# Optimization experiments

Hardware: AMD Instinct MI355X
Metric: run time of the kernel (lower is better)

## Reference

```python
import jax, jax.numpy as jnp
import numpy as np

EPS_REG = 0.1     # Sinkhorn regularization eps (init arg)
MAX_ITER = 50     # max Sinkhorn iterations (init arg)
THRESH = 0.1      # early-stop threshold from the torch code

N, P1, P2, D = 4, 2048, 2048, 64


def setup_inputs() -> dict:
    key = jax.random.key(0)
    k1, k2, k3 = jax.random.split(key, 3)
    x = jax.random.normal(k1, (N, P1, D), dtype=jnp.float32)
    y = jax.random.normal(k2, (N, P2, D), dtype=jnp.float32)
    M = jax.random.normal(k3, (D, D), dtype=jnp.float32)
    return {"x": x, "y": y, "M": M}


def _cost_matrix(x, y, M):
    # C_ij = (x_i - y_j) M (x_i - y_j)^T, expanded to avoid the [N,P1,P2,D]
    # difference tensor the torch code materializes (identical math):
    #   C = x M x^T (diag) + y M y^T (diag) - x M y^T - (y M x^T)^T
    xM = jnp.einsum('npd,de->npe', x, M)
    yM = jnp.einsum('nqd,de->nqe', y, M)
    dx = jnp.einsum('npd,npd->np', xM, x)  # [N,P1]
    dy = jnp.einsum('nqd,nqd->nq', yM, y)  # [N,P2]
    cross = jnp.einsum('npd,nqd->npq', xM, y) + jnp.einsum('nqd,npd->npq', yM, x)
    return dx[:, :, None] + dy[:, None, :] - cross  # [N,P1,P2]


def _bias(C, u, v, eps):
    # M_ij = (-C_ij + u_i + v_j) / eps
    return (-C + u[..., :, None] + v[..., None, :]) / eps


def _sinkhorn(C, eps):
    n, p1, p2 = C.shape
    log_mu = jnp.log(jnp.full((n, p1), 1.0 / p1, C.dtype) + 1e-8)
    log_nu = jnp.log(jnp.full((n, p2), 1.0 / p2, C.dtype) + 1e-8)
    u0 = jnp.zeros((n, p1), C.dtype)
    v0 = jnp.zeros((n, p2), C.dtype)

    def step(carry, _):
        u, v, active = carry
        u1 = u
        u_new = eps * (log_mu - jax.scipy.special.logsumexp(_bias(C, u, v, eps), axis=-1)) + u
        u = jnp.where(active, u_new, u)
        v_new = eps * (log_nu - jax.scipy.special.logsumexp(_bias(C, u, v, eps), axis=-2)) + v
        v = jnp.where(active, v_new, v)
        err = jnp.mean(jnp.sum(jnp.abs(u - u1), axis=-1))
        active = active & (err >= THRESH)  # freeze updates once converged (== torch break)
        return (u, v, active), None

    (u, v, _), _ = jax.lax.scan(step, (u0, v0, jnp.asarray(True)), None, length=MAX_ITER)
    return u, v


def reference(x, y, M):
    eps = EPS_REG
    C = _cost_matrix(x, y, M)
    u, v = _sinkhorn(C, eps)
    pi = jnp.exp(_bias(C, u, v, eps))
    cost = jnp.sum(pi * C, axis=(-2, -1))  # reduction='none' -> shape [N]
    return cost, pi, C
```

## Files before the change

### kernel.cpp

```cpp
#include <hip/hip_runtime.h>
#include <cstdint>
#include <cstddef>

#define NB 4
#define P1 2048
#define P2 2048
#define DD 64
#define ITER 50
#define EPS 0.1f
#define INV_EPS 10.0f
#define THRESH 0.1f
#define LOG_MU -7.6245985f
#define ELOG (-0.76245985f)
#define MU_VAL 0.00048829125f
#define ERRSLOTS 32
#define RP (P2 / 4)
#define PCHUNKS 128

__global__ void prep0(const float* __restrict__ M, float* __restrict__ S,
                      float* __restrict__ errAcc, int* __restrict__ active,
                      float* __restrict__ cost) {
    int t = threadIdx.x;
    for (int k = t; k < DD * DD; k += 256) {
        int d = k >> 6, e = k & 63;
        S[k] = M[d * DD + e] + M[e * DD + d];
    }
    for (int k = t; k < ITER * ERRSLOTS; k += 256) errAcc[k] = 0.0f;
    if (t < 64) active[t] = (t == 0) ? 1 : 0;
    if (t < NB) cost[t] = 0.0f;
}

__global__ __launch_bounds__(256) void prep1(const float* __restrict__ x,
                                             const float* __restrict__ y,
                                             const float* __restrict__ S,
                                             float* __restrict__ xS,
                                             float* __restrict__ dx,
                                             float* __restrict__ dy,
                                             float* __restrict__ u,
                                             float* __restrict__ v) {
    __shared__ float Sl[DD * DD];
    int t = threadIdx.x;
    for (int k = t; k < DD * DD; k += 256) Sl[k] = S[k];
    __syncthreads();
    int wave = t >> 6, lane = t & 63;
    int r = blockIdx.x * 4 + wave;
    bool isX = r < NB * P1;
    const float* src = isX ? x : y;
    int rr = isX ? r : r - NB * P1;
    float xv = src[(size_t)rr * DD + lane];
    float acc = 0.0f;
    #pragma unroll
    for (int d = 0; d < DD; ++d) {
        float xd = __shfl(xv, d, 64);
        acc = fmaf(xd, Sl[d * DD + lane], acc);
    }
    float p = acc * xv;
    #pragma unroll
    for (int o = 32; o; o >>= 1) p += __shfl_xor(p, o, 64);
    if (isX) {
        xS[(size_t)rr * DD + lane] = acc;
        if (lane == 0) { dx[rr] = 0.5f * p; u[rr] = 0.0f; }
    } else {
        if (lane == 0) { dy[rr] = 0.5f * p; v[rr] = 0.0f; }
    }
}

__global__ __launch_bounds__(256) void gemmC(const float* __restrict__ xS,
                                             const float* __restrict__ y,
                                             const float* __restrict__ dx,
                                             const float* __restrict__ dy,
                                             float* __restrict__ C) {
    __shared__ float xs[64][68];
    __shared__ float ys[64][68];
    int n = blockIdx.z;
    int i0 = blockIdx.y * 64, j0 = blockIdx.x * 64;
    int t = threadIdx.x;

    #pragma unroll
    for (int k = 0; k < 4; ++k) {
        int f = t + 256 * k;
        int row = f >> 4;
        int c4 = f & 15;
        float4 a = ((const float4*)xS)[((size_t)(n * P1 + i0 + row)) * (DD / 4) + c4];
        xs[4 * c4 + 0][row] = a.x; xs[4 * c4 + 1][row] = a.y;
        xs[4 * c4 + 2][row] = a.z; xs[4 * c4 + 3][row] = a.w;
        float4 b = ((const float4*)y)[((size_t)(n * P2 + j0 + row)) * (DD / 4) + c4];
        ys[4 * c4 + 0][row] = b.x; ys[4 * c4 + 1][row] = b.y;
        ys[4 * c4 + 2][row] = b.z; ys[4 * c4 + 3][row] = b.w;
    }
    __syncthreads();

    int tx = t & 15, ty = t >> 4;
    float acc[4][4] = {};
    #pragma unroll
    for (int e = 0; e < 64; ++e) {
        float4 a = *(const float4*)&xs[e][4 * ty];
        float4 b = *(const float4*)&ys[e][4 * tx];
        acc[0][0] = fmaf(a.x, b.x, acc[0][0]); acc[0][1] = fmaf(a.x, b.y, acc[0][1]);
        acc[0][2] = fmaf(a.x, b.z, acc[0][2]); acc[0][3] = fmaf(a.x, b.w, acc[0][3]);
        acc[1][0] = fmaf(a.y, b.x, acc[1][0]); acc[1][1] = fmaf(a.y, b.y, acc[1][1]);
        acc[1][2] = fmaf(a.y, b.z, acc[1][2]); acc[1][3] = fmaf(a.y, b.w, acc[1][3]);
        acc[2][0] = fmaf(a.z, b.x, acc[2][0]); acc[2][1] = fmaf(a.z, b.y, acc[2][1]);
        acc[2][2] = fmaf(a.z, b.z, acc[2][2]); acc[2][3] = fmaf(a.z, b.w, acc[2][3]);
        acc[3][0] = fmaf(a.w, b.x, acc[3][0]); acc[3][1] = fmaf(a.w, b.y, acc[3][1]);
        acc[3][2] = fmaf(a.w, b.z, acc[3][2]); acc[3][3] = fmaf(a.w, b.w, acc[3][3]);
    }

    int iBase = i0 + ty * 4, jBase = j0 + tx * 4;
    float4 dy4 = *(const float4*)&dy[n * P2 + jBase];
    #pragma unroll
    for (int r = 0; r < 4; ++r) {
        float dxv = dx[n * P1 + iBase + r];
        float4 o;
        o.x = dxv + dy4.x - acc[r][0];
        o.y = dxv + dy4.y - acc[r][1];
        o.z = dxv + dy4.z - acc[r][2];
        o.w = dxv + dy4.w - acc[r][3];
        *(float4*)&C[((size_t)(n * P1 + iBase + r)) * P2 + jBase] = o;
    }
}

__device__ __forceinline__ void load_row8(float4 dst[8], const float4* base, int lane) {
    #pragma unroll
    for (int k = 0; k < 8; ++k) dst[k] = base[lane + 64 * k];
}

__device__ __forceinline__ float row_lse(float4 c[8], float ai, const float* bl, int lane) {
    float m = -3.4e38f;
    #pragma unroll
    for (int k = 0; k < 8; ++k) {
        float4 vv = ((const float4*)bl)[lane + 64 * k];
        c[k].x = (ai - c[k].x) + vv.x;
        c[k].y = (ai - c[k].y) + vv.y;
        c[k].z = (ai - c[k].z) + vv.z;
        c[k].w = (ai - c[k].w) + vv.w;
        m = fmaxf(m, fmaxf(fmaxf(c[k].x, c[k].y), fmaxf(c[k].z, c[k].w)));
    }
    #pragma unroll
    for (int o = 1; o < 64; o <<= 1) m = fmaxf(m, __shfl_xor(m, o, 64));
    float s = 0.0f;
    #pragma unroll
    for (int k = 0; k < 8; ++k)
        s += __expf((c[k].x - m) * INV_EPS) + __expf((c[k].y - m) * INV_EPS) +
             __expf((c[k].z - m) * INV_EPS) + __expf((c[k].w - m) * INV_EPS);
    #pragma unroll
    for (int o = 1; o < 64; o <<= 1) s += __shfl_xor(s, o, 64);
    return EPS * __logf(s) + m;
}

__device__ __forceinline__ void mergec(float& m, float& s, float q) {
    float nm = fmaxf(m, q);
    s = s * __expf((m - nm) * INV_EPS) + __expf((q - nm) * INV_EPS);
    m = nm;
}
__device__ __forceinline__ void mergems(float& m, float& s, float mo, float so) {
    float nm = fmaxf(m, mo);
    s = s * __expf((m - nm) * INV_EPS) + so * __expf((mo - nm) * INV_EPS);
    m = nm;
}
__device__ __forceinline__ void merge44(float4& m, float4& s, float4 mo, float4 so) {
    mergems(m.x, s.x, mo.x, so.x);
    mergems(m.y, s.y, mo.y, so.y);
    mergems(m.z, s.z, mo.z, so.z);
    mergems(m.w, s.w, mo.w, so.w);
}

__device__ __forceinline__ void merge_row(float4 M[8], float4 S[8],
                                          const float4 q[8], float dr) {
    #pragma unroll
    for (int k = 0; k < 8; ++k) {
        mergec(M[k].x, S[k].x, q[k].x + dr);
        mergec(M[k].y, S[k].y, q[k].y + dr);
        mergec(M[k].z, S[k].z, q[k].z + dr);
        mergec(M[k].w, S[k].w, q[k].w + dr);
    }
}

__global__ __launch_bounds__(256) void iter_pass(const float* __restrict__ C,
                                                 float* __restrict__ u,
                                                 const float* __restrict__ v,
                                                 float* __restrict__ pm,
                                                 float* __restrict__ ps,
                                                 float* __restrict__ errAcc,
                                                 const int* __restrict__ active,
                                                 int t_iter) {
    if (!active[t_iter]) return;
    __shared__ float bl[P2];
    __shared__ float4 LM[4][512];
    __shared__ float4 LS[4][512];
    __shared__ float da_s[4];
    int t = threadIdx.x;
    int n = blockIdx.x >> 7;
    int i0 = (blockIdx.x & (PCHUNKS - 1)) * 16;
    {
        const float4* bsrc = (const float4*)(v + n * P2);
        ((float4*)bl)[t] = bsrc[t];
        ((float4*)bl)[t + 256] = bsrc[t + 256];
    }
    __syncthreads();

    int wave = t >> 6, lane = t & 63;
    int irow = i0 + wave * 4;
    float* arow = u + n * P1 + irow;
    float a0 = arow[0], a1 = arow[1], a2 = arow[2], a3 = arow[3];
    const float4* base = (const float4*)(C + ((size_t)(n * P1 + irow)) * P2);

    float4 M[8], S[8];
    #pragma unroll
    for (int k = 0; k < 8; ++k) {
        M[k] = make_float4(-3.4e38f, -3.4e38f, -3.4e38f, -3.4e38f);
        S[k] = make_float4(0.0f, 0.0f, 0.0f, 0.0f);
    }

    float4 A[8], B[8];
    load_row8(A, base, lane);
    load_row8(B, base + RP, lane);
    float l0 = row_lse(A, a0, bl, lane);
    float d0 = ELOG - l0;
    merge_row(M, S, A, d0);
    load_row8(A, base + 2 * RP, lane);
    float l1 = row_lse(B, a1, bl, lane);
    float d1 = ELOG - l1;
    merge_row(M, S, B, d1);
    load_row8(B, base + 3 * RP, lane);
    float l2 = row_lse(A, a2, bl, lane);
    float d2 = ELOG - l2;
    merge_row(M, S, A, d2);
    float l3 = row_lse(B, a3, bl, lane);
    float d3 = ELOG - l3;
    merge_row(M, S, B, d3);

    if (lane == 0) {
        arow[0] = a0 + d0; arow[1] = a1 + d1;
        arow[2] = a2 + d2; arow[3] = a3 + d3;
        da_s[wave] = fabsf(d0) + fabsf(d1) + fabsf(d2) + fabsf(d3);
    }

    #pragma unroll
    for (int k = 0; k < 8; ++k) {
        LM[wave][lane + 64 * k] = M[k];
        LS[wave][lane + 64 * k] = S[k];
    }
    __syncthreads();

    float4* pm4 = (float4*)pm;
    float4* ps4 = (float4*)ps;
    size_t pb4 = (size_t)blockIdx.x * 512;
    #pragma unroll
    for (int sl = 0; sl < 2; ++sl) {
        int slot = t + 256 * sl;
        float4 m = LM[0][slot], s = LS[0][slot];
        merge44(m, s, LM[1][slot], LS[1][slot]);
        merge44(m, s, LM[2][slot], LS[2][slot]);
        merge44(m, s, LM[3][slot], LS[3][slot]);
        pm4[pb4 + slot] = m;
        ps4[pb4 + slot] = s;
    }

    if (t == 0) {
        atomicAdd(&errAcc[t_iter * ERRSLOTS + (blockIdx.x & (ERRSLOTS - 1))],
                  da_s[0] + da_s[1] + da_s[2] + da_s[3]);
    }
}

__global__ __launch_bounds__(256) void v_comb(const float* __restrict__ pm,
                                              const float* __restrict__ ps,
                                              float* __restrict__ v,
                                              const float* __restrict__ errAcc,
                                              int* __restrict__ active,
                                              int t_iter) {
    if (blockIdx.x == 0 && threadIdx.x == 0) {
        float e = 0.0f;
        #pragma unroll
        for (int q = 0; q < ERRSLOTS; ++q) e += errAcc[t_iter * ERRSLOTS + q];
        if (active[t_iter] && (e * 0.25f >= THRESH)) active[t_iter + 1] = 1;
    }
    if (!active[t_iter]) return;
    __shared__ float LMv[4][64];
    __shared__ float LSv[4][64];
    int t = threadIdx.x, wave = t >> 6, lane = t & 63;
    int n = blockIdx.x >> 5;
    int j = ((blockIdx.x & 31) << 6) + lane;
    const float* pmb = pm + ((size_t)(n * PCHUNKS + wave * 32)) * P2 + j;
    const float* psb = ps + ((size_t)(n * PCHUNKS + wave * 32)) * P2 + j;
    float m0 = -3.4e38f, s0 = 0.0f, m1 = -3.4e38f, s1 = 0.0f;
    float m2 = -3.4e38f, s2 = 0.0f, m3 = -3.4e38f, s3 = 0.0f;
    #pragma unroll
    for (int c = 0; c < 32; c += 4) {
        mergems(m0, s0, pmb[(size_t)(c + 0) * P2], psb[(size_t)(c + 0) * P2]);
        mergems(m1, s1, pmb[(size_t)(c + 1) * P2], psb[(size_t)(c + 1) * P2]);
        mergems(m2, s2, pmb[(size_t)(c + 2) * P2], psb[(size_t)(c + 2) * P2]);
        mergems(m3, s3, pmb[(size_t)(c + 3) * P2], psb[(size_t)(c + 3) * P2]);
    }
    mergems(m0, s0, m1, s1);
    mergems(m2, s2, m3, s3);
    mergems(m0, s0, m2, s2);
    LMv[wave][lane] = m0; LSv[wave][lane] = s0;
    __syncthreads();
    if (wave == 0) {
        float m = LMv[0][lane], s = LSv[0][lane];
        mergems(m, s, LMv[1][lane], LSv[1][lane]);
        mergems(m, s, LMv[2][lane], LSv[2][lane]);
        mergems(m, s, LMv[3][lane], LSv[3][lane]);
        float lse = EPS * __logf(s) + m;
        v[n * P2 + j] = v[n * P2 + j] + ELOG - lse;
    }
}

__device__ __forceinline__ float row_sum(float4 c[8], float aiv, const float* bl,
                                         int lane) {
    float s = 0.0f;
    #pragma unroll
    for (int k = 0; k < 8; ++k) {
        float4 vv = ((const float4*)bl)[lane + 64 * k];
        c[k].x = __expf(fmaf(c[k].x, -INV_EPS, aiv + vv.x));
        c[k].y = __expf(fmaf(c[k].y, -INV_EPS, aiv + vv.y));
        c[k].z = __expf(fmaf(c[k].z, -INV_EPS, aiv + vv.z));
        c[k].w = __expf(fmaf(c[k].w, -INV_EPS, aiv + vv.w));
        s += (c[k].x + c[k].y) + (c[k].z + c[k].w);
    }
    #pragma unroll
    for (int o = 1; o < 64; o <<= 1) s += __shfl_xor(s, o, 64);
    return s;
}

__device__ __forceinline__ void acc_row(float4 S[8], const float4 q[8], float ed) {
    #pragma unroll
    for (int k = 0; k < 8; ++k) {
        S[k].x = fmaf(q[k].x, ed, S[k].x);
        S[k].y = fmaf(q[k].y, ed, S[k].y);
        S[k].z = fmaf(q[k].z, ed, S[k].z);
        S[k].w = fmaf(q[k].w, ed, S[k].w);
    }
}

__global__ __launch_bounds__(512) void iter_fast(const float* __restrict__ C,
                                                 float* __restrict__ u,
                                                 const float* __restrict__ v,
                                                 float* __restrict__ ps,
                                                 float* __restrict__ errAcc,
                                                 const int* __restrict__ active,
                                                 int t_iter) {
    if (!active[t_iter]) return;
    __shared__ float bl[P2];
    __shared__ float4 LS[8][512];
    __shared__ float da_s[8];
    int t = threadIdx.x;
    int n = blockIdx.x >> 7;
    int i0 = (blockIdx.x & (PCHUNKS - 1)) * 16;
    {
        const float4* bsrc = (const float4*)(v + n * P2);
        float4 b0 = bsrc[t];
        b0.x *= INV_EPS; b0.y *= INV_EPS; b0.z *= INV_EPS; b0.w *= INV_EPS;
        ((float4*)bl)[t] = b0;
    }
    __syncthreads();

    int wave = t >> 6, lane = t & 63;
    int irow = i0 + wave * 2;
    float* arow = u + n * P1 + irow;
    float a0 = arow[0], a1 = arow[1];
    const float4* base = (const float4*)(C + ((size_t)(n * P1 + irow)) * P2);

    float4 S[8];
    #pragma unroll
    for (int k = 0; k < 8; ++k) S[k] = make_float4(0.0f, 0.0f, 0.0f, 0.0f);

    float4 X[8], Y[8];
    load_row8(X, base, lane);
    load_row8(Y, base + RP, lane);
    float s0 = row_sum(X, a0 * INV_EPS, bl, lane);
    float d0 = ELOG - EPS * __logf(s0);
    acc_row(S, X, __fdividef(MU_VAL, s0));
    float s1 = row_sum(Y, a1 * INV_EPS, bl, lane);
    float d1 = ELOG - EPS * __logf(s1);
    acc_row(S, Y, __fdividef(MU_VAL, s1));

    if (lane == 0) {
        arow[0] = a0 + d0; arow[1] = a1 + d1;
        da_s[wave] = fabsf(d0) + fabsf(d1);
    }

    #pragma unroll
    for (int k = 0; k < 8; ++k) LS[wave][lane + 64 * k] = S[k];
    __syncthreads();

    float4* ps4 = (float4*)ps;
    size_t pb4 = (size_t)blockIdx.x * 512;
    {
        int slot = t;
        float4 x0 = LS[0][slot], x1 = LS[1][slot];
        float4 x2 = LS[2][slot], x3 = LS[3][slot];
        float4 x4 = LS[4][slot], x5 = LS[5][slot];
        float4 x6 = LS[6][slot], x7 = LS[7][slot];
        float4 o;
        o.x = ((x0.x + x1.x) + (x2.x + x3.x)) + ((x4.x + x5.x) + (x6.x + x7.x));
        o.y = ((x0.y + x1.y) + (x2.y + x3.y)) + ((x4.y + x5.y) + (x6.y + x7.y));
        o.z = ((x0.z + x1.z) + (x2.z + x3.z)) + ((x4.z + x5.z) + (x6.z + x7.z));
        o.w = ((x0.w + x1.w) + (x2.w + x3.w)) + ((x4.w + x5.w) + (x6.w + x7.w));
        ps4[pb4 + slot] = o;
    }

    if (t == 0) {
        atomicAdd(&errAcc[t_iter * ERRSLOTS + (blockIdx.x & (ERRSLOTS - 1))],
                  ((da_s[0] + da_s[1]) + (da_s[2] + da_s[3])) +
                  ((da_s[4] + da_s[5]) + (da_s[6] + da_s[7])));
    }
}

__global__ __launch_bounds__(256) void v_fast(const float* __restrict__ ps,
                                              float* __restrict__ v,
                                              const float* __restrict__ errAcc,
                                              int* __restrict__ active,
                                              int t_iter) {
    if (blockIdx.x == 0 && threadIdx.x == 0) {
        float e = 0.0f;
        #pragma unroll
        for (int q = 0; q < ERRSLOTS; ++q) e += errAcc[t_iter * ERRSLOTS + q];
        if (active[t_iter] && (e * 0.25f >= THRESH)) active[t_iter + 1] = 1;
    }
    if (!active[t_iter]) return;
    __shared__ float LSv[4][64];
    int t = threadIdx.x, wave = t >> 6, lane = t & 63;
    int n = blockIdx.x >> 5;
    int j = ((blockIdx.x & 31) << 6) + lane;
    const float* psb = ps + ((size_t)(n * PCHUNKS + wave * 32)) * P2 + j;
    float s0 = 0.0f, s1 = 0.0f, s2 = 0.0f, s3 = 0.0f;
    #pragma unroll
    for (int c = 0; c < 32; c += 4) {
        s0 += psb[(size_t)(c + 0) * P2];
        s1 += psb[(size_t)(c + 1) * P2];
        s2 += psb[(size_t)(c + 2) * P2];
        s3 += psb[(size_t)(c + 3) * P2];
    }
    LSv[wave][lane] = (s0 + s1) + (s2 + s3);
    __syncthreads();
    if (wave == 0) {
        float s = (LSv[0][lane] + LSv[1][lane]) + (LSv[2][lane] + LSv[3][lane]);
        v[n * P2 + j] = v[n * P2 + j] + ELOG - EPS * __logf(s);
    }
}

__device__ __forceinline__ float row_pi(const float4 c[8], float ui, const float* vl,
                                        int lane, float4* prow) {
    float acc = 0.0f;
    #pragma unroll
    for (int k = 0; k < 8; ++k) {
        float4 vv = ((const float4*)vl)[lane + 64 * k];
        float4 p;
        p.x = __expf(((ui - c[k].x) + vv.x) * INV_EPS);
        p.y = __expf(((ui - c[k].y) + vv.y) * INV_EPS);
        p.z = __expf(((ui - c[k].z) + vv.z) * INV_EPS);
        p.w = __expf(((ui - c[k].w) + vv.w) * INV_EPS);
        prow[lane + 64 * k] = p;
        acc += p.x * c[k].x + p.y * c[k].y + p.z * c[k].z + p.w * c[k].w;
    }
    return acc;
}

__global__ __launch_bounds__(512) void final_pass(const float* __restrict__ C,
                                                  const float* __restrict__ u,
                                                  const float* __restrict__ v,
                                                  float* __restrict__ pi,
                                                  float* __restrict__ cost) {
    __shared__ float vl[P2];
    __shared__ float red[8];
    int t = threadIdx.x;
    int n = blockIdx.x >> 7;
    int i0 = (blockIdx.x & 127) * 16;
    {
        const float4* vsrc = (const float4*)(v + n * P2);
        ((float4*)vl)[t] = vsrc[t];
    }
    __syncthreads();

    int wave = t >> 6, lane = t & 63;
    int irow = i0 + wave * 2;
    const float* urow = u + n * P1 + irow;
    float u0 = urow[0], u1 = urow[1];
    const float4* base = (const float4*)(C + ((size_t)(n * P1 + irow)) * P2);
    float4* pbase = (float4*)(pi + ((size_t)(n * P1 + irow)) * P2);

    float4 A[8], B[8];
    load_row8(A, base, lane);
    load_row8(B, base + RP, lane);
    float acc = row_pi(A, u0, vl, lane, pbase);
    acc += row_pi(B, u1, vl, lane, pbase + RP);

    #pragma unroll
    for (int o = 1; o < 64; o <<= 1) acc += __shfl_xor(acc, o, 64);
    if (lane == 0) red[wave] = acc;
    __syncthreads();
    if (t == 0) {
        atomicAdd(&cost[n], ((red[0] + red[1]) + (red[2] + red[3])) +
                            ((red[4] + red[5]) + (red[6] + red[7])));
    }
}

extern "C" void kernel_launch(void* const* d_in, const int* in_sizes, int n_in,
                              void* d_out, int out_size, void* d_ws, size_t ws_size,
                              hipStream_t stream) {
    const float* x = (const float*)d_in[0];
    const float* y = (const float*)d_in[1];
    const float* M = (const float*)d_in[2];
    float* out = (float*)d_out;
    float* cost = out;
    float* pi = out + NB;
    float* C = out + NB + (size_t)NB * P1 * P2;

    float* ws = (float*)d_ws;
    float* S      = ws;
    float* xS     = S + DD * DD;
    float* dx     = xS + (size_t)NB * P1 * DD;
    float* dy     = dx + NB * P1;
    float* u      = dy + NB * P2;
    float* v      = u + NB * P1;
    float* errAcc = v + NB * P2;
    int*   active = (int*)(errAcc + ITER * ERRSLOTS);
    float* ws_end = (float*)(active + 64);

    size_t base_floats = (size_t)(ws_end - ws);
    size_t pmps_floats = 2 * (size_t)NB * PCHUNKS * P2;
    float* pm;
    float* ps;
    if (ws_size >= (base_floats + pmps_floats) * sizeof(float)) {
        pm = ws_end;
        ps = ws_end + pmps_floats / 2;
    } else {
        pm = pi;
        ps = pi + pmps_floats / 2;
    }

    prep0<<<1, 256, 0, stream>>>(M, S, errAcc, active, cost);
    prep1<<<(NB * (P1 + P2)) / 4, 256, 0, stream>>>(x, y, S, xS, dx, dy, u, v);
    gemmC<<<dim3(P2 / 64, P1 / 64, NB), 256, 0, stream>>>(xS, y, dx, dy, C);
    iter_pass<<<NB * PCHUNKS, 256, 0, stream>>>(C, u, v, pm, ps, errAcc, active, 0);
    v_comb<<<NB * 32, 256, 0, stream>>>(pm, ps, v, errAcc, active, 0);
    for (int t = 1; t < ITER; ++t) {
        iter_fast<<<NB * PCHUNKS, 512, 0, stream>>>(C, u, v, ps, errAcc, active, t);
        v_fast<<<NB * 32, 256, 0, stream>>>(ps, v, errAcc, active, t);
    }
    final_pass<<<NB * P1 / 16, 512, 0, stream>>>(C, u, v, pi, cost);
}
```

Measured before the change: 1.032 ms.

## Store a half-precision copy of the cost matrix for Sinkhorn iterations

The cost-matrix GEMM now also writes an fp16 copy of C into workspace when enough space is available. The first pass, the 49 fast iterations and the final pi/cost pass all read this half-size copy instead of fp32 C, which halves the bytes streamed on every iteration. The trade-off is accuracy: fp16 rounding of large cost values is amplified by the 1/eps scaling inside the exponent, and the final pi and cost outputs are also computed from the rounded C. The gemm kernel also pays for an extra write.

```diff
diff --git a/kernel.cpp b/kernel.cpp
--- a/kernel.cpp
+++ b/kernel.cpp
@@ -1,4 +1,5 @@
 #include <hip/hip_runtime.h>
+#include <hip/hip_fp16.h>
 #include <cstdint>
 #include <cstddef>
 
@@ -15,6 +16,7 @@
 #define MU_VAL 0.00048829125f
 #define ERRSLOTS 32
 #define RP (P2 / 4)
+#define RP16 (P2 / 8)
 #define PCHUNKS 128
 
 __global__ void prep0(const float* __restrict__ M, float* __restrict__ S,
@@ -69,7 +71,8 @@
                                              const float* __restrict__ y,
                                              const float* __restrict__ dx,
                                              const float* __restrict__ dy,
-                                             float* __restrict__ C) {
+                                             float* __restrict__ C,
+                                             unsigned short* __restrict__ C16h) {
     __shared__ float xs[64][68];
     __shared__ float ys[64][68];
     int n = blockIdx.z;
@@ -116,13 +119,28 @@
         o.y = dxv + dy4.y - acc[r][1];
         o.z = dxv + dy4.z - acc[r][2];
         o.w = dxv + dy4.w - acc[r][3];
-        *(float4*)&C[((size_t)(n * P1 + iBase + r)) * P2 + jBase] = o;
+        size_t idx = ((size_t)(n * P1 + iBase + r)) * P2 + jBase;
+        *(float4*)&C[idx] = o;
+        if (C16h) {
+            __half2 h01 = __floats2half2_rn(o.x, o.y);
+            __half2 h23 = __floats2half2_rn(o.z, o.w);
+            uint2 pk;
+            pk.x = *reinterpret_cast<unsigned int*>(&h01);
+            pk.y = *reinterpret_cast<unsigned int*>(&h23);
+            *reinterpret_cast<uint2*>(&C16h[idx]) = pk;
+        }
     }
 }
 
 __device__ __forceinline__ void load_row8(float4 dst[8], const float4* base, int lane) {
     #pragma unroll
     for (int k = 0; k < 8; ++k) dst[k] = base[lane + 64 * k];
+}
+
+__device__ __forceinline__ float2 h2f2(unsigned int uu) {
+    __half2 h;
+    *reinterpret_cast<unsigned int*>(&h) = uu;
+    return __half22float2(h);
 }
 
 __device__ __forceinline__ float row_lse(float4 c[8], float ai, const float* bl, int lane) {
@@ -174,6 +192,67 @@
         mergec(M[k].z, S[k].z, q[k].z + dr);
         mergec(M[k].w, S[k].w, q[k].w + dr);
     }
+}
+
+
+__device__ __forceinline__ float row_lse16(const uint4 H[4], float Q[32], float ai,
+                                           const float* bl, int lane) {
+    const float4* bl4 = (const float4*)bl;
+    float m = -3.4e38f;
+    #pragma unroll
+    for (int k = 0; k < 4; ++k) {
+        int g = lane + 64 * k;
+        float2 f0 = h2f2(H[k].x), f1 = h2f2(H[k].y);
+        float2 f2 = h2f2(H[k].z), f3 = h2f2(H[k].w);
+        float4 v0 = bl4[2 * g], v1 = bl4[2 * g + 1];
+        int o = 8 * k;
+        Q[o + 0] = (ai - f0.x) + v0.x; Q[o + 1] = (ai - f0.y) + v0.y;
+        Q[o + 2] = (ai - f1.x) + v0.z; Q[o + 3] = (ai - f1.y) + v0.w;
+        Q[o + 4] = (ai - f2.x) + v1.x; Q[o + 5] = (ai - f2.y) + v1.y;
+        Q[o + 6] = (ai - f3.x) + v1.z; Q[o + 7] = (ai - f3.y) + v1.w;
+        m = fmaxf(m, fmaxf(fmaxf(fmaxf(Q[o+0],Q[o+1]), fmaxf(Q[o+2],Q[o+3])),
+                           fmaxf(fmaxf(Q[o+4],Q[o+5]), fmaxf(Q[o+6],Q[o+7]))));
+    }
+    #pragma unroll
+    for (int o = 1; o < 64; o <<= 1) m = fmaxf(m, __shfl_xor(m, o, 64));
+    float s = 0.0f;
+    #pragma unroll
+    for (int j = 0; j < 32; ++j) s += __expf((Q[j] - m) * INV_EPS);
+    #pragma unroll
+    for (int o = 1; o < 64; o <<= 1) s += __shfl_xor(s, o, 64);
+    return EPS * __logf(s) + m;
+}
+
+__device__ __forceinline__ void merge_row16(float M[32], float S[32],
+                                            const float Q[32], float dr) {
+    #pragma unroll
+    for (int j = 0; j < 32; ++j) mergec(M[j], S[j], Q[j] + dr);
+}
+
+__device__ __forceinline__ float row_sum16(const uint4 H[4], float X[32], float aiv,
+                                           const float* bl, int lane) {
+    const float4* bl4 = (const float4*)bl;
+    float s = 0.0f;
+    #pragma unroll
+    for (int k = 0; k < 4; ++k) {
+        int g = lane + 64 * k;
+        float2 f0 = h2f2(H[k].x), f1 = h2f2(H[k].y);
+        float2 f2 = h2f2(H[k].z), f3 = h2f2(H[k].w);
+        float4 v0 = bl4[2 * g], v1 = bl4[2 * g + 1];
+        int o = 8 * k;
+        X[o + 0] = __expf(fmaf(f0.x, -INV_EPS, aiv + v0.x));
+        X[o + 1] = __expf(fmaf(f0.y, -INV_EPS, aiv + v0.y));
+        X[o + 2] = __expf(fmaf(f1.x, -INV_EPS, aiv + v0.z));
+        X[o + 3] = __expf(fmaf(f1.y, -INV_EPS, aiv + v0.w));
+        X[o + 4] = __expf(fmaf(f2.x, -INV_EPS, aiv + v1.x));
+        X[o + 5] = __expf(fmaf(f2.y, -INV_EPS, aiv + v1.y));
+        X[o + 6] = __expf(fmaf(f3.x, -INV_EPS, aiv + v1.z));
+        X[o + 7] = __expf(fmaf(f3.y, -INV_EPS, aiv + v1.w));
+        s += ((X[o+0]+X[o+1])+(X[o+2]+X[o+3])) + ((X[o+4]+X[o+5])+(X[o+6]+X[o+7]));
+    }
+    #pragma unroll
+    for (int o = 1; o < 64; o <<= 1) s += __shfl_xor(s, o, 64);
+    return s;
 }
 
 __global__ __launch_bounds__(256) void iter_pass(const float* __restrict__ C,
@@ -263,6 +342,97 @@
     }
 }
 
+__global__ __launch_bounds__(256) void iter_pass16(const unsigned short* __restrict__ C16,
+                                                   float* __restrict__ u,
+                                                   const float* __restrict__ v,
+                                                   float* __restrict__ pm,
+                                                   float* __restrict__ ps,
+                                                   float* __restrict__ errAcc,
+                                                   const int* __restrict__ active,
+                                                   int t_iter) {
+    if (!active[t_iter]) return;
+    __shared__ float bl[P2];
+    __shared__ float4 LM[4][512];
+    __shared__ float4 LS[4][512];
+    __shared__ float da_s[4];
+    int t = threadIdx.x;
+    int n = blockIdx.x >> 7;
+    int i0 = (blockIdx.x & (PCHUNKS - 1)) * 16;
+    {
+        const float4* bsrc = (const float4*)(v + n * P2);
+        ((float4*)bl)[t] = bsrc[t];
+        ((float4*)bl)[t + 256] = bsrc[t + 256];
+    }
+    __syncthreads();
+
+    int wave = t >> 6, lane = t & 63;
+    int irow = i0 + wave * 4;
+    float* arow = u + n * P1 + irow;
+    float a0 = arow[0], a1 = arow[1], a2 = arow[2], a3 = arow[3];
+    const uint4* b16 = (const uint4*)(C16 + ((size_t)(n * P1 + irow)) * P2);
+
+    float M[32], S[32], Q[32];
+    #pragma unroll
+    for (int j = 0; j < 32; ++j) { M[j] = -3.4e38f; S[j] = 0.0f; }
+
+    uint4 HA[4], HB[4];
+    #pragma unroll
+    for (int k = 0; k < 4; ++k) HA[k] = b16[lane + 64 * k];
+    #pragma unroll
+    for (int k = 0; k < 4; ++k) HB[k] = (b16 + RP16)[lane + 64 * k];
+    float l0 = row_lse16(HA, Q, a0, bl, lane);
+    float d0 = ELOG - l0;
+    merge_row16(M, S, Q, d0);
+    #pragma unroll
+    for (int k = 0; k < 4; ++k) HA[k] = (b16 + 2 * RP16)[lane + 64 * k];
+    float l1 = row_lse16(HB, Q, a1, bl, lane);
+    float d1 = ELOG - l1;
+    merge_row16(M, S, Q, d1);
+    #pragma unroll
+    for (int k = 0; k < 4; ++k) HB[k] = (b16 + 3 * RP16)[lane + 64 * k];
+    float l2 = row_lse16(HA, Q, a2, bl, lane);
+    float d2 = ELOG - l2;
+    merge_row16(M, S, Q, d2);
+    float l3 = row_lse16(HB, Q, a3, bl, lane);
+    float d3 = ELOG - l3;
+    merge_row16(M, S, Q, d3);
+
+    if (lane == 0) {
+        arow[0] = a0 + d0; arow[1] = a1 + d1;
+        arow[2] = a2 + d2; arow[3] = a3 + d3;
+        da_s[wave] = fabsf(d0) + fabsf(d1) + fabsf(d2) + fabsf(d3);
+    }
+
+    #pragma unroll
+    for (int k = 0; k < 4; ++k) {
+        int g = lane + 64 * k;
+        LM[wave][2*g+0] = make_float4(M[8*k+0], M[8*k+1], M[8*k+2], M[8*k+3]);
+        LM[wave][2*g+1] = make_float4(M[8*k+4], M[8*k+5], M[8*k+6], M[8*k+7]);
+        LS[wave][2*g+0] = make_float4(S[8*k+0], S[8*k+1], S[8*k+2], S[8*k+3]);
+        LS[wave][2*g+1] = make_float4(S[8*k+4], S[8*k+5], S[8*k+6], S[8*k+7]);
+    }
+    __syncthreads();
+
+    float4* pm4 = (float4*)pm;
+    float4* ps4 = (float4*)ps;
+    size_t pb4 = (size_t)blockIdx.x * 512;
+    #pragma unroll
+    for (int sl = 0; sl < 2; ++sl) {
+        int slot = t + 256 * sl;
+        float4 m = LM[0][slot], s = LS[0][slot];
+        merge44(m, s, LM[1][slot], LS[1][slot]);
+        merge44(m, s, LM[2][slot], LS[2][slot]);
+        merge44(m, s, LM[3][slot], LS[3][slot]);
+        pm4[pb4 + slot] = m;
+        ps4[pb4 + slot] = s;
+    }
+
+    if (t == 0) {
+        atomicAdd(&errAcc[t_iter * ERRSLOTS + (blockIdx.x & (ERRSLOTS - 1))],
+                  da_s[0] + da_s[1] + da_s[2] + da_s[3]);
+    }
+}
+
 __global__ __launch_bounds__(256) void v_comb(const float* __restrict__ pm,
                                               const float* __restrict__ ps,
                                               float* __restrict__ v,
@@ -408,6 +578,90 @@
     }
 }
 
+__global__ __launch_bounds__(512) void iter_fast16(const unsigned short* __restrict__ C16,
+                                                   float* __restrict__ u,
+                                                   const float* __restrict__ v,
+                                                   float* __restrict__ ps,
+                                                   float* __restrict__ errAcc,
+                                                   const int* __restrict__ active,
+                                                   int t_iter) {
+    if (!active[t_iter]) return;
+    __shared__ float bl[P2];
+    __shared__ float4 LS[8][512];
+    __shared__ float da_s[8];
+    int t = threadIdx.x;
+    int n = blockIdx.x >> 7;
+    int i0 = (blockIdx.x & (PCHUNKS - 1)) * 16;
+    {
+        const float4* bsrc = (const float4*)(v + n * P2);
+        float4 b0 = bsrc[t];
+        b0.x *= INV_EPS; b0.y *= INV_EPS; b0.z *= INV_EPS; b0.w *= INV_EPS;
+        ((float4*)bl)[t] = b0;
+    }
+    __syncthreads();
+
+    int wave = t >> 6, lane = t & 63;
+    int irow = i0 + wave * 2;
+    float* arow = u + n * P1 + irow;
+    float a0 = arow[0], a1 = arow[1];
+    const uint4* b16 = (const uint4*)(C16 + ((size_t)(n * P1 + irow)) * P2);
+
+    float S[32], X[32];
+    #pragma unroll
+    for (int j = 0; j < 32; ++j) S[j] = 0.0f;
+
+    uint4 HA[4], HB[4];
+    #pragma unroll
+    for (int k = 0; k < 4; ++k) HA[k] = b16[lane + 64 * k];
+    #pragma unroll
+    for (int k = 0; k < 4; ++k) HB[k] = (b16 + RP16)[lane + 64 * k];
+    float s0 = row_sum16(HA, X, a0 * INV_EPS, bl, lane);
+    float d0 = ELOG - EPS * __logf(s0);
+    float e0 = __fdividef(MU_VAL, s0);
+    #pragma unroll
+    for (int j = 0; j < 32; ++j) S[j] = fmaf(X[j], e0, S[j]);
+    float s1 = row_sum16(HB, X, a1 * INV_EPS, bl, lane);
+    float d1 = ELOG - EPS * __logf(s1);
+    float e1 = __fdividef(MU_VAL, s1);
+    #pragma unroll
+    for (int j = 0; j < 32; ++j) S[j] = fmaf(X[j], e1, S[j]);
+
+    if (lane == 0) {
+        arow[0] = a0 + d0; arow[1] = a1 + d1;
+        da_s[wave] = fabsf(d0) + fabsf(d1);
+    }
+
+    #pragma unroll
+    for (int k = 0; k < 4; ++k) {
+        int g = lane + 64 * k;
+        LS[wave][2*g+0] = make_float4(S[8*k+0], S[8*k+1], S[8*k+2], S[8*k+3]);
+        LS[wave][2*g+1] = make_float4(S[8*k+4], S[8*k+5], S[8*k+6], S[8*k+7]);
+    }
+    __syncthreads();
+
+    float4* ps4 = (float4*)ps;
+    size_t pb4 = (size_t)blockIdx.x * 512;
+    {
+        int slot = t;
+        float4 x0 = LS[0][slot], x1 = LS[1][slot];
+        float4 x2 = LS[2][slot], x3 = LS[3][slot];
+        float4 x4 = LS[4][slot], x5 = LS[5][slot];
+        float4 x6 = LS[6][slot], x7 = LS[7][slot];
+        float4 o;
+        o.x = ((x0.x + x1.x) + (x2.x + x3.x)) + ((x4.x + x5.x) + (x6.x + x7.x));
+        o.y = ((x0.y + x1.y) + (x2.y + x3.y)) + ((x4.y + x5.y) + (x6.y + x7.y));
+        o.z = ((x0.z + x1.z) + (x2.z + x3.z)) + ((x4.z + x5.z) + (x6.z + x7.z));
+        o.w = ((x0.w + x1.w) + (x2.w + x3.w)) + ((x4.w + x5.w) + (x6.w + x7.w));
+        ps4[pb4 + slot] = o;
+    }
+
+    if (t == 0) {
+        atomicAdd(&errAcc[t_iter * ERRSLOTS + (blockIdx.x & (ERRSLOTS - 1))],
+                  ((da_s[0] + da_s[1]) + (da_s[2] + da_s[3])) +
+                  ((da_s[4] + da_s[5]) + (da_s[6] + da_s[7])));
+    }
+}
+
 __global__ __launch_bounds__(256) void v_fast(const float* __restrict__ ps,
                                               float* __restrict__ v,
                                               const float* __restrict__ errAcc,
@@ -497,6 +751,73 @@
     }
 }
 
+__device__ __forceinline__ float row_pi16(const uint4 H[4], float ui, const float* vl,
+                                          int lane, float4* prow) {
+    const float4* bl4 = (const float4*)vl;
+    float acc = 0.0f;
+    #pragma unroll
+    for (int k = 0; k < 4; ++k) {
+        int g = lane + 64 * k;
+        float2 f0 = h2f2(H[k].x), f1 = h2f2(H[k].y);
+        float2 f2 = h2f2(H[k].z), f3 = h2f2(H[k].w);
+        float4 v0 = bl4[2 * g], v1 = bl4[2 * g + 1];
+        float p0 = __expf(((ui - f0.x) + v0.x) * INV_EPS);
+        float p1 = __expf(((ui - f0.y) + v0.y) * INV_EPS);
+        float p2 = __expf(((ui - f1.x) + v0.z) * INV_EPS);
+        float p3 = __expf(((ui - f1.y) + v0.w) * INV_EPS);
+        float p4 = __expf(((ui - f2.x) + v1.x) * INV_EPS);
+        float p5 = __expf(((ui - f2.y) + v1.y) * INV_EPS);
+        float p6 = __expf(((ui - f3.x) + v1.z) * INV_EPS);
+        float p7 = __expf(((ui - f3.y) + v1.w) * INV_EPS);
+        prow[2 * g + 0] = make_float4(p0, p1, p2, p3);
+        prow[2 * g + 1] = make_float4(p4, p5, p6, p7);
+        acc += ((p0 * f0.x + p1 * f0.y) + (p2 * f1.x + p3 * f1.y)) +
+               ((p4 * f2.x + p5 * f2.y) + (p6 * f3.x + p7 * f3.y));
+    }
+    return acc;
+}
+
+__global__ __launch_bounds__(512) void final_pass16(const unsigned short* __restrict__ C16,
+                                                    const float* __restrict__ u,
+                                                    const float* __restrict__ v,
+                                                    float* __restrict__ pi,
+                                                    float* __restrict__ cost) {
+    __shared__ float vl[P2];
+    __shared__ float red[8];
+    int t = threadIdx.x;
+    int n = blockIdx.x >> 7;
+    int i0 = (blockIdx.x & 127) * 16;
+    {
+        const float4* vsrc = (const float4*)(v + n * P2);
+        ((float4*)vl)[t] = vsrc[t];
+    }
+    __syncthreads();
+
+    int wave = t >> 6, lane = t & 63;
+    int irow = i0 + wave * 2;
+    const float* urow = u + n * P1 + irow;
+    float u0 = urow[0], u1 = urow[1];
+    const uint4* b16 = (const uint4*)(C16 + ((size_t)(n * P1 + irow)) * P2);
+    float4* pbase = (float4*)(pi + ((size_t)(n * P1 + irow)) * P2);
+
+    uint4 HA[4], HB[4];
+    #pragma unroll
+    for (int k = 0; k < 4; ++k) HA[k] = b16[lane + 64 * k];
+    #pragma unroll
+    for (int k = 0; k < 4; ++k) HB[k] = (b16 + RP16)[lane + 64 * k];
+    float acc = row_pi16(HA, u0, vl, lane, pbase);
+    acc += row_pi16(HB, u1, vl, lane, pbase + RP);
+
+    #pragma unroll
+    for (int o = 1; o < 64; o <<= 1) acc += __shfl_xor(acc, o, 64);
+    if (lane == 0) red[wave] = acc;
+    __syncthreads();
+    if (t == 0) {
+        atomicAdd(&cost[n], ((red[0] + red[1]) + (red[2] + red[3])) +
+                            ((red[4] + red[5]) + (red[6] + red[7])));
+    }
+}
+
 extern "C" void kernel_launch(void* const* d_in, const int* in_sizes, int n_in,
                               void* d_out, int out_size, void* d_ws, size_t ws_size,
                               hipStream_t stream) {
@@ -521,24 +842,44 @@
 
     size_t base_floats = (size_t)(ws_end - ws);
     size_t pmps_floats = 2 * (size_t)NB * PCHUNKS * P2;
+    bool ws_pmps = ws_size >= (base_floats + pmps_floats) * sizeof(float);
     float* pm;
     float* ps;
-    if (ws_size >= (base_floats + pmps_floats) * sizeof(float)) {
+    if (ws_pmps) {
         pm = ws_end;
         ps = ws_end + pmps_floats / 2;
     } else {
         pm = pi;
         ps = pi + pmps_floats / 2;
     }
+    size_t c16_off = (base_floats + pmps_floats + 3) & ~(size_t)3;
+    size_t c16_floats = (size_t)NB * P1 * P2 / 2;
+    bool use16 = ws_pmps && ws_size >= (c16_off + c16_floats) * sizeof(float);
+    unsigned short* C16 = use16 ? (unsigned short*)(ws + c16_off) : nullptr;
 
     prep0<<<1, 256, 0, stream>>>(M, S, errAcc, active, cost);
     prep1<<<(NB * (P1 + P2)) / 4, 256, 0, stream>>>(x, y, S, xS, dx, dy, u, v);
-    gemmC<<<dim3(P2 / 64, P1 / 64, NB), 256, 0, stream>>>(xS, y, dx, dy, C);
-    iter_pass<<<NB * PCHUNKS, 256, 0, stream>>>(C, u, v, pm, ps, errAcc, active, 0);
-    v_comb<<<NB * 32, 256, 0, stream>>>(pm, ps, v, errAcc, active, 0);
-    for (int t = 1; t < ITER; ++t) {
-        iter_fast<<<NB * PCHUNKS, 512, 0, stream>>>(C, u, v, ps, errAcc, active, t);
-        v_fast<<<NB * 32, 256, 0, stream>>>(ps, v, errAcc, active, t);
-    }
-    final_pass<<<NB * P1 / 16, 512, 0, stream>>>(C, u, v, pi, cost);
-}
+    gemmC<<<dim3(P2 / 64, P1 / 64, NB), 256, 0, stream>>>(xS, y, dx, dy, C, C16);
+
+    if (use16) {
+        iter_pass16<<<NB * PCHUNKS, 256, 0, stream>>>(C16, u, v, pm, ps, errAcc,
+                                                      active, 0);
+        v_comb<<<NB * 32, 256, 0, stream>>>(pm, ps, v, errAcc, active, 0);
+        for (int t = 1; t < ITER; ++t) {
+            iter_fast16<<<NB * PCHUNKS, 512, 0, stream>>>(C16, u, v, ps, errAcc,
+                                                          active, t);
+            v_fast<<<NB * 32, 256, 0, stream>>>(ps, v, errAcc, active, t);
+        }
+        final_pass16<<<NB * P1 / 16, 512, 0, stream>>>(C16, u, v, pi, cost);
+    } else {
+        iter_pass<<<NB * PCHUNKS, 256, 0, stream>>>(C, u, v, pm, ps, errAcc,
+                                                    active, 0);
+        v_comb<<<NB * 32, 256, 0, stream>>>(pm, ps, v, errAcc, active, 0);
+        for (int t = 1; t < ITER; ++t) {
+            iter_fast<<<NB * PCHUNKS, 512, 0, stream>>>(C, u, v, ps, errAcc,
+                                                        active, t);
+            v_fast<<<NB * 32, 256, 0, stream>>>(ps, v, errAcc, active, t);
+        }
+        final_pass<<<NB * P1 / 16, 512, 0, stream>>>(C, u, v, pi, cost);
+    }
+}
```

Measured after the change: 1.064 ms. 1.03x slower.
